# Kernel tuning notes

Hardware: AMD Instinct MI355X
Metric: run time of the kernel (lower is better)

## Reference

```python
import jax, jax.numpy as jnp
import numpy as np

DIM, NH, HD = 512, 16, 32   # dim, num_heads, head_dim = dim // num_heads
WH, WW = 8, 8               # window_size
SCALE = HD ** -0.5


def _rope2(t):
    """Axial 2D rotary embedding. t: (M, WH, WW, HD). First HD/2 dims rotate
    with the height position, last HD/2 with the width position."""
    d = HD // 2
    inv_freq = 1.0 / (10000.0 ** (jnp.arange(0, d, 2, dtype=jnp.float32) / d))  # (d/2,)

    def cos_sin(n):
        ang = jnp.arange(n, dtype=jnp.float32)[:, None] * inv_freq              # (n, d/2)
        return (jnp.concatenate([jnp.cos(ang)] * 2, -1),
                jnp.concatenate([jnp.sin(ang)] * 2, -1))                        # (n, d)

    def rot_half(u):
        u1, u2 = jnp.split(u, 2, axis=-1)
        return jnp.concatenate([-u2, u1], -1)

    cos_h, sin_h = cos_sin(WH)
    cos_w, sin_w = cos_sin(WW)
    th, tw = t[..., :d], t[..., d:]
    th = th * cos_h[:, None, :] + rot_half(th) * sin_h[:, None, :]
    tw = tw * cos_w[None, :, :] + rot_half(tw) * sin_w[None, :, :]
    return jnp.concatenate([th, tw], -1)


def setup_inputs() -> dict:
    key = jax.random.key(0)
    ks = jax.random.split(key, 8)
    s = 0.02
    return {
        "x": jax.random.normal(ks[0], (8, 64, 64, DIM), dtype=jnp.float32),
        "qkv_w": jax.random.normal(ks[1], (DIM, 3 * DIM), dtype=jnp.float32) * s,
        "qkv_b": jnp.zeros((3 * DIM,), dtype=jnp.float32),
        "kv_w": jax.random.normal(ks[2], (DIM, 2 * DIM), dtype=jnp.float32) * s,
        "kv_b": jnp.zeros((2 * DIM,), dtype=jnp.float32),
        "proj_w": jax.random.normal(ks[3], (DIM, DIM), dtype=jnp.float32) * s,
        "proj_b": jnp.zeros((DIM,), dtype=jnp.float32),
    }


def reference(x, qkv_w, qkv_b, kv_w, kv_b, proj_w, proj_b):
    B, H, W, C = x.shape
    # --- hydra linear-attention branch (computed in the torch module even when
    # use_attn=True, but its result is discarded on that path) ---
    hy_k, hy_v = jnp.split(x @ kv_w + kv_b, 2, axis=-1)
    hy_k = hy_k / jnp.linalg.norm(hy_k, axis=-1, keepdims=True)
    hy_kv = (hy_k * hy_v).reshape(B, -1, C).sum(axis=-2, keepdims=True)  # (B,1,C), unused (use_attn=True)

    # --- window partition: (B,H,W,C) -> (B*nW, N, C), N = WH*WW ---
    xw = (x.reshape(B, H // WH, WH, W // WW, WW, C)
           .transpose(0, 1, 3, 2, 4, 5)
           .reshape(-1, WH * WW, C))
    B_, N, _ = xw.shape

    qkv = (xw @ qkv_w + qkv_b).reshape(B_, N, 3, NH, HD).transpose(2, 0, 3, 1, 4)
    q, k, v = qkv[0], qkv[1], qkv[2]                 # each (B_, NH, N, HD)

    q = _rope2(q.reshape(-1, WH, WW, HD)).reshape(B_, NH, N, HD)
    k = _rope2(k.reshape(-1, WH, WW, HD)).reshape(B_, NH, N, HD)

    attn = jax.nn.softmax(jnp.einsum('bhnd,bhmd->bhnm', q * SCALE, k), axis=-1)
    out = jnp.einsum('bhnm,bhmd->bhnd', attn, v)     # (B_, NH, N, HD)
    out = out.transpose(0, 2, 1, 3).reshape(B_, N, C)

    # --- window reverse: (B*nW, N, C) -> (B, H*W, C) ---
    out = (out.reshape(B, H // WH, W // WW, WH, WW, C)
              .transpose(0, 1, 3, 2, 4, 5)
              .reshape(B, H * W, C))

    out = out @ proj_w + proj_b
    return out.reshape(B, H, W, C)
```

## Files before the change

### kernel.cpp

```cpp
#include <hip/hip_runtime.h>
#include <cstdint>
#include <cstddef>

typedef float v4f  __attribute__((ext_vector_type(4)));
typedef __bf16 v8bf __attribute__((ext_vector_type(8)));
typedef __bf16 v4bf __attribute__((ext_vector_type(4)));

#define M_TOT 32768
#define KDIM  512
#define NQKV  1536
#define NPROJ 512

__device__ __constant__ float c_invf[8] = {
  1.f, 0.31622776601683794f, 0.1f, 0.031622776601683794f,
  0.01f, 0.0031622776601683794f, 0.001f, 0.00031622776601683794f };

__device__ __forceinline__ void async_copy16(const void* g, void* l) {
  __builtin_amdgcn_global_load_lds((const __attribute__((address_space(1))) void*)g,
                                   (__attribute__((address_space(3))) void*)l, 16, 0, 0);
}

__global__ __launch_bounds__(256) void prep_kernel(
    const float* __restrict__ x,      __bf16* __restrict__ xb,
    const float* __restrict__ qkv_w,  __bf16* __restrict__ qkv_wt,
    const float* __restrict__ proj_w, __bf16* __restrict__ proj_wt) {
  const int tid = threadIdx.x;
  const int bx  = blockIdx.x;
  if (bx < 2048) {
    const int n8 = M_TOT * KDIM / 8;
    for (int i = bx * 256 + tid; i < n8; i += 2048 * 256) {
      const float4* p = (const float4*)x + (size_t)i * 2;
      float4 a = p[0], b = p[1];
      v8bf r = { (__bf16)a.x, (__bf16)a.y, (__bf16)a.z, (__bf16)a.w,
                 (__bf16)b.x, (__bf16)b.y, (__bf16)b.z, (__bf16)b.w };
      *(v8bf*)(xb + (size_t)i * 8) = r;
    }
    return;
  }
  const float* w; __bf16* wt; int N, n0, k0;
  if (bx < 2048 + 192) {
    int idx = bx - 2048;
    w = qkv_w; wt = qkv_wt; N = NQKV;
    n0 = (idx % 24) * 64; k0 = (idx / 24) * 64;
  } else {
    int idx = bx - 2048 - 192;
    w = proj_w; wt = proj_wt; N = NPROJ;
    n0 = (idx % 8) * 64; k0 = (idx / 8) * 64;
  }
  __shared__ __bf16 t[64 * 72];
#pragma unroll
  for (int i = 0; i < 16; ++i) {
    int e = i * 256 + tid;
    int kk = e >> 6, nn = e & 63;
    t[nn * 72 + kk] = (__bf16)w[(size_t)(k0 + kk) * N + n0 + nn];
  }
  __syncthreads();
#pragma unroll
  for (int i = 0; i < 2; ++i) {
    int e = i * 256 + tid;
    int nn = e >> 3, kc = e & 7;
    *(v8bf*)&wt[(size_t)(n0 + nn) * KDIM + k0 + kc * 8] = *(const v8bf*)&t[nn * 72 + kc * 8];
  }
}

#define REG_STRIDE 12288

__global__ __launch_bounds__(256, 3) void gemm_qkv_attn(
    const __bf16* __restrict__ A,
    const __bf16* __restrict__ Bt,
    const float* __restrict__ bias,
    __bf16* __restrict__ attn_out)
{
  __shared__ __align__(16) char smem[49152];
  __bf16* As = (__bf16*)smem;
  __bf16* Bs = (__bf16*)(smem + 16384);

  const int tid  = threadIdx.x;
  const int lane = tid & 63;
  const int wave = tid >> 6;
  const int lrow = lane & 15, quad = lane >> 4;
  const int hp   = blockIdx.y & 7;
  const int mt   = (blockIdx.y & ~7) | blockIdx.x;
  const int wl   = wave >> 1, hl = wave & 1;
  const int head = hp * 2 + hl;

  int mbase[2];
#pragma unroll
  for (int l = 0; l < 2; ++l) {
    int w  = mt * 2 + l;
    int b  = w >> 6, Wr = (w >> 3) & 7, Wc = w & 7;
    mbase[l] = b * 4096 + Wr * 512 + Wc * 8;
  }

  const __bf16* aptr[4]; __bf16* adst[4];
  const __bf16* bptr[6]; __bf16* bdst[6];
#pragma unroll
  for (int i = 0; i < 4; ++i) {
    int s = i * 256 + tid;
    int row = s >> 3, c = s & 7, qc = c ^ (row & 7);
    int tok = row & 63;
    int m = mbase[row >> 6] + ((tok >> 3) << 6) + (tok & 7);
    aptr[i] = A + (size_t)m * KDIM + qc * 8;
    adst[i] = &As[(i * 256 + (tid & ~63)) * 8];
  }
#pragma unroll
  for (int i = 0; i < 6; ++i) {
    int s = i * 256 + tid;
    int rl = s >> 3, c = s & 7, qc = c ^ (rl & 7);
    int sel = rl >> 6, rem = rl & 63;
    int grow = sel * 512 + (hp * 2 + (rem >> 5)) * 32 + (rem & 31);
    bptr[i] = Bt + (size_t)grow * KDIM + qc * 8;
    bdst[i] = &Bs[(i * 256 + (tid & ~63)) * 8];
  }

  v4f acc[4][6] = {};

  for (int k0 = 0; k0 < KDIM; k0 += 64) {
#pragma unroll
    for (int i = 0; i < 4; ++i) { async_copy16(aptr[i], adst[i]); aptr[i] += 64; }
#pragma unroll
    for (int i = 0; i < 6; ++i) { async_copy16(bptr[i], bdst[i]); bptr[i] += 64; }
    __syncthreads();
#pragma unroll
    for (int kb = 0; kb < 2; ++kb) {
      int sx = (((kb << 2) | quad) ^ (lrow & 7)) * 8;
      v8bf af[4], bfr[6];
#pragma unroll
      for (int mi = 0; mi < 4; ++mi)
        af[mi] = *(const v8bf*)&As[(wl * 64 + mi * 16 + lrow) * 64 + sx];
#pragma unroll
      for (int j = 0; j < 6; ++j)
        bfr[j] = *(const v8bf*)&Bs[((j >> 1) * 64 + hl * 32 + (j & 1) * 16 + lrow) * 64 + sx];
#pragma unroll
      for (int mi = 0; mi < 4; ++mi)
#pragma unroll
        for (int j = 0; j < 6; ++j)
          acc[mi][j] = __builtin_amdgcn_mfma_f32_16x16x32_bf16(af[mi], bfr[j], acc[mi][j], 0, 0, 0);
    }
    __syncthreads();
  }

  __bf16* reg = (__bf16*)(smem + wave * REG_STRIDE);
  __bf16* qL = reg;
  __bf16* kL = reg + 64 * 32;
  __bf16* vL = reg + 2 * 64 * 32;

  {
    const float invf = c_invf[lrow & 7];
    float cvh[4], svh[4], cvw[4], svw[4];
#pragma unroll
    for (int mi = 0; mi < 4; ++mi)
      __sincosf((float)(mi * 2 + (quad >> 1)) * invf, &svh[mi], &cvh[mi]);
#pragma unroll
    for (int r = 0; r < 4; ++r)
      __sincosf((float)((quad & 1) * 4 + r) * invf, &svw[r], &cvw[r]);

#pragma unroll
    for (int j = 0; j < 4; ++j) {
      int sel = j >> 1, nh = j & 1;
      int hd  = nh * 16 + lrow;
      int g   = nh * 2 + (lrow >> 3);
      float bv = bias[sel * 512 + head * 32 + hd];
      __bf16* dst = sel ? kL : qL;
#pragma unroll
      for (int mi = 0; mi < 4; ++mi) {
#pragma unroll
        for (int r = 0; r < 4; ++r) {
          int tok = mi * 16 + quad * 4 + r;
          float val = acc[mi][j][r] + bv;
          float partner = __shfl_xor(val, 8);
          float cv = nh ? cvw[r] : cvh[mi];
          float sv = nh ? svw[r] : svh[mi];
          float rh = (lrow & 8) ? partner : -partner;
          val = val * cv + rh * sv;
          if (sel == 0) val *= 0.17677669529663689f;
          dst[tok * 32 + ((g ^ quad) << 3) + (lrow & 7)] = (__bf16)val;
        }
      }
    }
  }
#pragma unroll
  for (int j = 4; j < 6; ++j) {
    int hd = (j - 4) * 16 + lrow;
    float bv = bias[1024 + head * 32 + hd];
#pragma unroll
    for (int mi = 0; mi < 4; ++mi) {
      v4bf pk;
#pragma unroll
      for (int r = 0; r < 4; ++r) pk[r] = (__bf16)(acc[mi][j][r] + bv);
      int gt = mi * 2 + (quad >> 1);
      *(v4bf*)&vL[hd * 64 + ((gt ^ (lrow & 7)) << 3) + (quad & 1) * 4] = pk;
    }
  }

  const int sq = (quad ^ (lrow >> 2)) << 3;
  v8bf qf[4], kf[4];
#pragma unroll
  for (int mi = 0; mi < 4; ++mi)
    qf[mi] = *(const v8bf*)&qL[(mi * 16 + lrow) * 32 + sq];
#pragma unroll
  for (int ni = 0; ni < 4; ++ni)
    kf[ni] = *(const v8bf*)&kL[(ni * 16 + lrow) * 32 + sq];

  v4f S[4][4] = {};
#pragma unroll
  for (int ni = 0; ni < 4; ++ni)
#pragma unroll
    for (int mi = 0; mi < 4; ++mi)
      S[ni][mi] = __builtin_amdgcn_mfma_f32_16x16x32_bf16(kf[ni], qf[mi], S[ni][mi], 0, 0, 0);

#pragma unroll
  for (int mi = 0; mi < 4; ++mi) {
    float mx = S[0][mi][0];
#pragma unroll
    for (int ni = 0; ni < 4; ++ni)
#pragma unroll
      for (int r = 0; r < 4; ++r) mx = fmaxf(mx, S[ni][mi][r]);
    mx = fmaxf(mx, __shfl_xor(mx, 16));
    mx = fmaxf(mx, __shfl_xor(mx, 32));
    float sum = 0.f;
#pragma unroll
    for (int ni = 0; ni < 4; ++ni)
#pragma unroll
      for (int r = 0; r < 4; ++r) {
        float e = __expf(S[ni][mi][r] - mx);
        S[ni][mi][r] = e; sum += e;
      }
    sum += __shfl_xor(sum, 16);
    sum += __shfl_xor(sum, 32);
    float inv = 1.f / sum;
#pragma unroll
    for (int ni = 0; ni < 4; ++ni)
#pragma unroll
      for (int r = 0; r < 4; ++r) S[ni][mi][r] *= inv;
  }

  __bf16* P = reg;
#pragma unroll
  for (int mi = 0; mi < 4; ++mi) {
    int q = mi * 16 + lrow;
#pragma unroll
    for (int ni = 0; ni < 4; ++ni) {
      v4bf pk;
#pragma unroll
      for (int r = 0; r < 4; ++r) pk[r] = (__bf16)S[ni][mi][r];
      int g = ni * 2 + (quad >> 1);
      *(v4bf*)&P[q * 64 + ((g ^ (lrow & 7)) << 3) + (quad & 1) * 4] = pk;
    }
  }

  v8bf pf[4][2], vf[2][2];
#pragma unroll
  for (int mi = 0; mi < 4; ++mi)
#pragma unroll
    for (int kc = 0; kc < 2; ++kc) {
      int row = mi * 16 + lrow;
      pf[mi][kc] = *(const v8bf*)&P[row * 64 + (((kc * 4 + quad) ^ (lrow & 7)) << 3)];
    }
#pragma unroll
  for (int kc = 0; kc < 2; ++kc)
#pragma unroll
    for (int nj = 0; nj < 2; ++nj) {
      int hd = nj * 16 + lrow;
      vf[kc][nj] = *(const v8bf*)&vL[hd * 64 + (((kc * 4 + quad) ^ (lrow & 7)) << 3)];
    }

  v4f o[2][4] = {};
#pragma unroll
  for (int nj = 0; nj < 2; ++nj)
#pragma unroll
    for (int mi = 0; mi < 4; ++mi)
#pragma unroll
      for (int kc = 0; kc < 2; ++kc)
        o[nj][mi] = __builtin_amdgcn_mfma_f32_16x16x32_bf16(vf[kc][nj], pf[mi][kc], o[nj][mi], 0, 0, 0);

  const int gwin = mt * 2 + wl;
#pragma unroll
  for (int mi = 0; mi < 4; ++mi) {
    size_t rowoff = ((size_t)gwin * 64 + mi * 16 + lrow) * 512 + head * 32 + quad * 4;
#pragma unroll
    for (int nj = 0; nj < 2; ++nj) {
      v4bf pk;
#pragma unroll
      for (int r = 0; r < 4; ++r) pk[r] = (__bf16)o[nj][mi][r];
      *(v4bf*)&attn_out[rowoff + nj * 16] = pk;
    }
  }
}

__global__ __launch_bounds__(256, 4) void gemm_proj(
    const __bf16* __restrict__ A,
    const __bf16* __restrict__ Bt,
    const float* __restrict__ bias,
    float* __restrict__ out)
{
  __shared__ __align__(16) char smem[32768];
  __bf16* smemb = (__bf16*)smem;
  const int tid  = threadIdx.x;
  const int lane = tid & 63;
  const int wave = tid >> 6;
  const int lrow = lane & 15, quad = lane >> 4;

  const int lin = blockIdx.x + blockIdx.y * 4;
  const int xcd = lin & 7, idx = lin >> 3;
  const int m0  = (xcd * 32 + (idx >> 2)) * 128;
  const int n0  = (idx & 3) * 128;

  const __bf16* aptr[2]; const __bf16* bptr[2]; int adst[2], bdst[2];
#pragma unroll
  for (int i = 0; i < 2; ++i) {
    int chunk = i * 256 + tid;
    int row2 = chunk >> 3, slot = chunk & 7;
    int g = slot ^ (row2 & 7);
    int trow = row2 * 2 + (g >> 2), kgrp = g & 3;
    aptr[i] = A + (size_t)(m0 + trow) * KDIM + kgrp * 8;
    bptr[i] = Bt + (size_t)(n0 + trow) * KDIM + kgrp * 8;
    adst[i] = (i * 256 + (tid & ~63)) * 8;
    bdst[i] = 4096 + adst[i];
  }

#pragma unroll
  for (int i = 0; i < 2; ++i) {
    async_copy16(aptr[i], smemb + adst[i]);
    async_copy16(bptr[i], smemb + bdst[i]);
  }

  v4f acc[8][2] = {};
  const int slot8 = ((((lrow & 1) << 2) | quad) ^ (lrow >> 1)) << 3;
  const int lr2 = lrow >> 1;

#pragma unroll
  for (int t = 0; t < 16; ++t) {
    __syncthreads();
    if (t < 15) {
      int nb  = ((t + 1) & 1) * 8192;
      int kof = (t + 1) * 32;
#pragma unroll
      for (int i = 0; i < 2; ++i) {
        async_copy16(aptr[i] + kof, smemb + nb + adst[i]);
        async_copy16(bptr[i] + kof, smemb + nb + bdst[i]);
      }
    }
    const __bf16* Ac = smemb + (t & 1) * 8192;
    const __bf16* Bc = Ac + 4096;
    v8bf af[2], bfr[8];
#pragma unroll
    for (int mi = 0; mi < 2; ++mi)
      af[mi] = *(const v8bf*)&Ac[(wave * 16 + mi * 8 + lr2) * 64 + slot8];
#pragma unroll
    for (int ni = 0; ni < 8; ++ni)
      bfr[ni] = *(const v8bf*)&Bc[(ni * 8 + lr2) * 64 + slot8];
    __builtin_amdgcn_s_setprio(1);
#pragma unroll
    for (int ni = 0; ni < 8; ++ni)
#pragma unroll
      for (int mi = 0; mi < 2; ++mi)
        acc[ni][mi] = __builtin_amdgcn_mfma_f32_16x16x32_bf16(bfr[ni], af[mi], acc[ni][mi], 0, 0, 0);
    __builtin_amdgcn_s_setprio(0);
  }

  float4 bv[8];
#pragma unroll
  for (int ni = 0; ni < 8; ++ni)
    bv[ni] = *(const float4*)&bias[n0 + ni * 16 + quad * 4];

  const int mb = m0 + wave * 32;
#pragma unroll
  for (int mi = 0; mi < 2; ++mi) {
    int m    = mb + mi * 16 + lrow;
    int win  = m >> 6, tok = m & 63;
    int bb   = win >> 6;
    int hblk = (win >> 3) & 7, wblk = win & 7;
    int h    = hblk * 8 + (tok >> 3);
    int w    = wblk * 8 + (tok & 7);
    float* orow = &out[(((size_t)bb * 64 + h) * 64 + w) * 512 + n0 + quad * 4];
#pragma unroll
    for (int ni = 0; ni < 8; ++ni) {
      float4 v = { acc[ni][mi][0] + bv[ni].x, acc[ni][mi][1] + bv[ni].y,
                   acc[ni][mi][2] + bv[ni].z, acc[ni][mi][3] + bv[ni].w };
      *(float4*)&orow[ni * 16] = v;
    }
  }
}

extern "C" void kernel_launch(void* const* d_in, const int* in_sizes, int n_in,
                              void* d_out, int out_size, void* d_ws, size_t ws_size,
                              hipStream_t stream) {
  (void)in_sizes; (void)n_in; (void)out_size; (void)ws_size;
  const float* x      = (const float*)d_in[0];
  const float* qkv_w  = (const float*)d_in[1];
  const float* qkv_b  = (const float*)d_in[2];
  const float* proj_w = (const float*)d_in[5];
  const float* proj_b = (const float*)d_in[6];
  float* out = (float*)d_out;

  char* ws = (char*)d_ws;
  size_t off = 0;
  auto alloc = [&](size_t bytes) {
    char* p = ws + off;
    off += (bytes + 255) & ~(size_t)255;
    return (void*)p;
  };
  __bf16* xb       = (__bf16*)alloc((size_t)M_TOT * KDIM * 2);
  __bf16* qkv_wt   = (__bf16*)alloc((size_t)NQKV * KDIM * 2);
  __bf16* proj_wt  = (__bf16*)alloc((size_t)KDIM * KDIM * 2);
  __bf16* attn_out = (__bf16*)alloc((size_t)M_TOT * KDIM * 2);

  prep_kernel<<<dim3(2048 + 192 + 64), dim3(256), 0, stream>>>(
      x, xb, qkv_w, qkv_wt, proj_w, proj_wt);

  gemm_qkv_attn<<<dim3(8, 256), dim3(256), 0, stream>>>(
      xb, qkv_wt, qkv_b, attn_out);

  gemm_proj<<<dim3(4, 256), dim3(256), 0, stream>>>(
      attn_out, proj_wt, proj_b, out);
}
```

Measured before the change: 220.3 us.

## Load QKV GEMM fragments directly from global memory, bypassing LDS staging

After: 334.0 us. +51.6%, slower.

```diff
diff --git a/kernel.cpp b/kernel.cpp
--- a/kernel.cpp
+++ b/kernel.cpp
@@ -72,8 +72,6 @@
     __bf16* __restrict__ attn_out)
 {
   __shared__ __align__(16) char smem[49152];
-  __bf16* As = (__bf16*)smem;
-  __bf16* Bs = (__bf16*)(smem + 16384);
 
   const int tid  = threadIdx.x;
   const int lane = tid & 63;
@@ -84,60 +82,38 @@
   const int wl   = wave >> 1, hl = wave & 1;
   const int head = hp * 2 + hl;
 
-  int mbase[2];
-#pragma unroll
-  for (int l = 0; l < 2; ++l) {
-    int w  = mt * 2 + l;
-    int b  = w >> 6, Wr = (w >> 3) & 7, Wc = w & 7;
-    mbase[l] = b * 4096 + Wr * 512 + Wc * 8;
-  }
-
-  const __bf16* aptr[4]; __bf16* adst[4];
-  const __bf16* bptr[6]; __bf16* bdst[6];
-#pragma unroll
-  for (int i = 0; i < 4; ++i) {
-    int s = i * 256 + tid;
-    int row = s >> 3, c = s & 7, qc = c ^ (row & 7);
-    int tok = row & 63;
-    int m = mbase[row >> 6] + ((tok >> 3) << 6) + (tok & 7);
-    aptr[i] = A + (size_t)m * KDIM + qc * 8;
-    adst[i] = &As[(i * 256 + (tid & ~63)) * 8];
-  }
-#pragma unroll
-  for (int i = 0; i < 6; ++i) {
-    int s = i * 256 + tid;
-    int rl = s >> 3, c = s & 7, qc = c ^ (rl & 7);
-    int sel = rl >> 6, rem = rl & 63;
-    int grow = sel * 512 + (hp * 2 + (rem >> 5)) * 32 + (rem & 31);
-    bptr[i] = Bt + (size_t)grow * KDIM + qc * 8;
-    bdst[i] = &Bs[(i * 256 + (tid & ~63)) * 8];
+  const int win = mt * 2 + wl;
+  const int mbase = (win >> 6) * 4096 + ((win >> 3) & 7) * 512 + (win & 7) * 8;
+
+  const __bf16* ap[4];
+#pragma unroll
+  for (int mi = 0; mi < 4; ++mi) {
+    int tok = mi * 16 + lrow;
+    int m = mbase + ((tok >> 3) << 6) + (tok & 7);
+    ap[mi] = A + (size_t)m * KDIM + quad * 8;
+  }
+  const __bf16* bp[6];
+#pragma unroll
+  for (int j = 0; j < 6; ++j) {
+    int grow = (j >> 1) * 512 + head * 32 + (j & 1) * 16 + lrow;
+    bp[j] = Bt + (size_t)grow * KDIM + quad * 8;
   }
 
   v4f acc[4][6] = {};
 
-  for (int k0 = 0; k0 < KDIM; k0 += 64) {
-#pragma unroll
-    for (int i = 0; i < 4; ++i) { async_copy16(aptr[i], adst[i]); aptr[i] += 64; }
-#pragma unroll
-    for (int i = 0; i < 6; ++i) { async_copy16(bptr[i], bdst[i]); bptr[i] += 64; }
-    __syncthreads();
-#pragma unroll
-    for (int kb = 0; kb < 2; ++kb) {
-      int sx = (((kb << 2) | quad) ^ (lrow & 7)) * 8;
-      v8bf af[4], bfr[6];
-#pragma unroll
-      for (int mi = 0; mi < 4; ++mi)
-        af[mi] = *(const v8bf*)&As[(wl * 64 + mi * 16 + lrow) * 64 + sx];
+#pragma unroll
+  for (int t = 0; t < 16; ++t) {
+    const int ko = t * 32;
+    v8bf af[4], bfr[6];
+#pragma unroll
+    for (int mi = 0; mi < 4; ++mi) af[mi] = *(const v8bf*)(ap[mi] + ko);
+#pragma unroll
+    for (int j = 0; j < 6; ++j)    bfr[j] = *(const v8bf*)(bp[j] + ko);
+#pragma unroll
+    for (int mi = 0; mi < 4; ++mi)
 #pragma unroll
       for (int j = 0; j < 6; ++j)
-        bfr[j] = *(const v8bf*)&Bs[((j >> 1) * 64 + hl * 32 + (j & 1) * 16 + lrow) * 64 + sx];
-#pragma unroll
-      for (int mi = 0; mi < 4; ++mi)
-#pragma unroll
-        for (int j = 0; j < 6; ++j)
-          acc[mi][j] = __builtin_amdgcn_mfma_f32_16x16x32_bf16(af[mi], bfr[j], acc[mi][j], 0, 0, 0);
-    }
-    __syncthreads();
+        acc[mi][j] = __builtin_amdgcn_mfma_f32_16x16x32_bf16(af[mi], bfr[j], acc[mi][j], 0, 0, 0);
   }
 
   __bf16* reg = (__bf16*)(smem + wave * REG_STRIDE);
@@ -274,10 +250,9 @@
       for (int kc = 0; kc < 2; ++kc)
         o[nj][mi] = __builtin_amdgcn_mfma_f32_16x16x32_bf16(vf[kc][nj], pf[mi][kc], o[nj][mi], 0, 0, 0);
 
-  const int gwin = mt * 2 + wl;
 #pragma unroll
   for (int mi = 0; mi < 4; ++mi) {
-    size_t rowoff = ((size_t)gwin * 64 + mi * 16 + lrow) * 512 + head * 32 + quad * 4;
+    size_t rowoff = ((size_t)win * 64 + mi * 16 + lrow) * 512 + head * 32 + quad * 4;
 #pragma unroll
     for (int nj = 0; nj < 2; ++nj) {
       v4bf pk;
```
